# Performance work log

Measured on AMD Instinct MI355X. Metric: run time of the kernel, lower is better.

The kernel has to match this reference:

```python
import jax, jax.numpy as jnp
import numpy as np

B, S, D, H = 2, 2048, 1024, 16
DK = D // H
NEG = -1e9


def setup_inputs() -> dict:
    key = jax.random.key(0)
    ks = jax.random.split(key, 12)
    inp = {
        "query": jax.random.normal(ks[0], (B, S, D), jnp.float32),
        "key": jax.random.normal(ks[1], (B, S, D), jnp.float32),
        "value": jax.random.normal(ks[2], (B, S, D), jnp.float32),
        "mask": jax.random.randint(ks[3], (B, S), 0, 2, jnp.int32),
    }
    # 4 linears (q, k, v, out), each d_model x d_model with bias.
    scale = 1.0 / np.sqrt(D)
    for i, name in enumerate(["wq", "wk", "wv", "wo"]):
        inp[name] = jax.random.uniform(ks[4 + i], (D, D), jnp.float32, -scale, scale)
        inp["b" + name[1]] = jax.random.uniform(ks[8 + i], (D,), jnp.float32, -scale, scale)
    return inp


def _split_heads(x):  # [B,S,D] -> [B,H,S,DK]
    return x.reshape(B, S, H, DK).transpose(0, 2, 1, 3)


def reference(query, key, value, mask, wq, bq, wk, bk, wv, bv, wo, bo):
    q = _split_heads(query @ wq.T + bq)
    k = _split_heads(key @ wk.T + bk)
    v = _split_heads(value @ wv.T + bv)
    scores = jnp.einsum("bhqd,bhkd->bhqk", q, k) / jnp.sqrt(jnp.float32(DK))
    # mask: [B,S] -> [B,1,1,S]; masked_fill where mask == 0
    m = mask[:, None, None, :]
    scores = jnp.where(m == 0, NEG, scores)
    attn = jax.nn.softmax(scores, axis=-1)  # dropout p=0 (eval) -> identity
    x = jnp.einsum("bhqk,bhkd->bhqd", attn, v)
    x = x.transpose(0, 2, 1, 3).reshape(B, S, D)
    return x @ wo.T + bo
```

## Files before the change

kernel.cpp:

```cpp
#include <hip/hip_runtime.h>


typedef _Float16 f16;
typedef _Float16 f16x8 __attribute__((ext_vector_type(8)));
typedef _Float16 f16x4 __attribute__((ext_vector_type(4)));
typedef __fp16 fp16x2r __attribute__((ext_vector_type(2)));
typedef float f32x4 __attribute__((ext_vector_type(4)));
typedef float f32x16 __attribute__((ext_vector_type(16)));
typedef unsigned u32x2 __attribute__((ext_vector_type(2)));

#define MFMA_F16(a, b, c) __builtin_amdgcn_mfma_f32_16x16x32_f16((a), (b), (c), 0, 0, 0)
#define MFMA32(a, b, c) __builtin_amdgcn_mfma_f32_32x32x16_f16((a), (b), (c), 0, 0, 0)
#define L2E 1.44269504088896340736f

__device__ __forceinline__ void gld16(const void* g, void* l) {
    __builtin_amdgcn_global_load_lds(
        (__attribute__((address_space(1))) void*)(g),
        (__attribute__((address_space(3))) void*)(l), 16, 0, 0);
}

__device__ __forceinline__ void swap_halves(unsigned& a, unsigned& b) {
#if __has_builtin(__builtin_amdgcn_permlane32_swap)
    u32x2 r = __builtin_amdgcn_permlane32_swap(a, b, false, false);
    a = r[0];
    b = r[1];
#else
    unsigned pa = (unsigned)__shfl_xor((int)a, 32);
    unsigned pb = (unsigned)__shfl_xor((int)b, 32);
    if ((threadIdx.x & 32) == 0) { b = pa; } else { a = pb; }
#endif
}

__global__ __launch_bounds__(256) void cvt_kernel(
    const float* __restrict__ q, const float* __restrict__ k,
    const float* __restrict__ v,
    const float* __restrict__ wq, const float* __restrict__ wk,
    const float* __restrict__ wv, const float* __restrict__ wo,
    f16* __restrict__ oq, f16* __restrict__ ok, f16* __restrict__ ov,
    f16* __restrict__ owq, f16* __restrict__ owk, f16* __restrict__ owv,
    f16* __restrict__ owo)
{
    const int z = blockIdx.y;
    const float* src;
    f16* dst;
    int n;
    switch (z) {
        case 0: src = q;  dst = oq;  n = 4194304; break;
        case 1: src = k;  dst = ok;  n = 4194304; break;
        case 2: src = v;  dst = ov;  n = 4194304; break;
        case 3: src = wq; dst = owq; n = 1048576; break;
        case 4: src = wk; dst = owk; n = 1048576; break;
        case 5: src = wv; dst = owv; n = 1048576; break;
        default: src = wo; dst = owo; n = 1048576; break;
    }
    int idx = (blockIdx.x * 256 + threadIdx.x) * 8;
    if (idx >= n) return;
    float4 a = *(const float4*)(src + idx);
    float4 b = *(const float4*)(src + idx + 4);
    f16x8 h = { (f16)a.x, (f16)a.y, (f16)a.z, (f16)a.w,
                (f16)b.x, (f16)b.y, (f16)b.z, (f16)b.w };
    *(f16x8*)(dst + idx) = h;
}

__global__ __launch_bounds__(256) void proj_qkv_kernel(
    const f16* __restrict__ xq, const f16* __restrict__ xk,
    const f16* __restrict__ xv,
    const f16* __restrict__ wqh, const f16* __restrict__ wkh,
    const f16* __restrict__ wvh,
    const float* __restrict__ bq, const float* __restrict__ bk,
    const float* __restrict__ bv,
    f16* __restrict__ qh, f16* __restrict__ kh, f16* __restrict__ vt)
{
    const int z = blockIdx.z;
    const f16* X = (z == 0) ? xq : (z == 1) ? xk : xv;
    const f16* W = (z == 0) ? wqh : (z == 1) ? wkh : wvh;
    const float* bias = (z == 0) ? bq : (z == 1) ? bk : bv;
    const f16* P0 = (z < 2) ? W : X;
    const f16* P1 = (z < 2) ? X : W;

    __shared__ __align__(16) f16 smem[16384];
    f16* As = smem;
    f16* Bs = smem + 8192;
    f16* L  = smem;

    const int t = threadIdx.x;
    const int wave = t >> 6, lane = t & 63, quad = lane >> 4, l15 = lane & 15;
    const int m_base = (wave >> 1) * 64, n_base = (wave & 1) * 64;
    const int blockM = (z < 2) ? blockIdx.y * 128 : blockIdx.x * 128;
    const int blockN = (z < 2) ? blockIdx.x * 128 : blockIdx.y * 128;

    const int srow = lane >> 3;
    const int sblk = (lane & 7) ^ srow;

    f32x4 acc[4][4];
#pragma unroll
    for (int mt = 0; mt < 4; mt++)
#pragma unroll
        for (int nt = 0; nt < 4; nt++)
            acc[mt][nt] = (f32x4){0.f, 0.f, 0.f, 0.f};

    for (int k0 = 0; k0 < 1024; k0 += 64) {
        __syncthreads();
#pragma unroll
        for (int j = 0; j < 4; j++) {
            int r0 = wave * 32 + j * 8;
            gld16(&P0[(size_t)(blockM + r0 + srow) * 1024 + k0 + sblk * 8],
                  &As[r0 * 64]);
            gld16(&P1[(size_t)(blockN + r0 + srow) * 1024 + k0 + sblk * 8],
                  &Bs[r0 * 64]);
        }
        __syncthreads();

#pragma unroll
        for (int c = 0; c < 2; c++) {
            f16x8 af[4], bf[4];
#pragma unroll
            for (int mt = 0; mt < 4; mt++)
                af[mt] = *(const f16x8*)(&As[(m_base + mt * 16 + l15) * 64 +
                                             (((c * 4 + quad) ^ (l15 & 7)) << 3)]);
#pragma unroll
            for (int nt = 0; nt < 4; nt++)
                bf[nt] = *(const f16x8*)(&Bs[(n_base + nt * 16 + l15) * 64 +
                                             (((c * 4 + quad) ^ (l15 & 7)) << 3)]);
#pragma unroll
            for (int mt = 0; mt < 4; mt++)
#pragma unroll
                for (int nt = 0; nt < 4; nt++)
                    acc[mt][nt] = MFMA_F16(af[mt], bf[nt], acc[mt][nt]);
        }
    }

    if (z < 2) {
        f16* o = (z == 0) ? qh : kh;
        const float scale = (z == 0) ? 0.125f * L2E : 1.0f;
        float4 b4[4];
#pragma unroll
        for (int mt = 0; mt < 4; mt++)
            b4[mt] = *(const float4*)(&bias[blockM + m_base + mt * 16 + quad * 4]);

#pragma unroll
        for (int half = 0; half < 2; half++) {
            __syncthreads();
            if ((wave & 1) == half) {
#pragma unroll
                for (int mt = 0; mt < 4; mt++)
#pragma unroll
                    for (int nt = 0; nt < 4; nt++) {
                        f16x4 pk = {
                            (f16)((acc[mt][nt][0] + b4[mt].x) * scale),
                            (f16)((acc[mt][nt][1] + b4[mt].y) * scale),
                            (f16)((acc[mt][nt][2] + b4[mt].z) * scale),
                            (f16)((acc[mt][nt][3] + b4[mt].w) * scale) };
                        *(f16x4*)(&L[(nt * 16 + l15) * 136 +
                                     m_base + mt * 16 + quad * 4]) = pk;
                    }
            }
            __syncthreads();
#pragma unroll
            for (int pass = 0; pass < 4; pass++) {
                int unit = pass * 32 + (t >> 3);
                int hh = unit >> 6, s_loc = unit & 63;
                f16x8 vv = *(const f16x8*)(&L[s_loc * 136 + hh * 64 + (t & 7) * 8]);
                int s_glob = blockN + half * 64 + s_loc;
                int b = s_glob >> 11, s = s_glob & 2047;
                int h_glob = (blockM >> 6) + hh;
                *(f16x8*)(&o[(((size_t)(b * 16 + h_glob) * 2048 + s) << 6) +
                             (t & 7) * 8]) = vv;
            }
        }
    } else {
        float bv_[4];
#pragma unroll
        for (int nt = 0; nt < 4; nt++)
            bv_[nt] = bias[blockN + n_base + nt * 16 + l15];

#pragma unroll
        for (int half = 0; half < 2; half++) {
            __syncthreads();
            if ((wave & 1) == half) {
#pragma unroll
                for (int mt = 0; mt < 4; mt++)
#pragma unroll
                    for (int nt = 0; nt < 4; nt++) {
                        f16x4 pk = { (f16)(acc[mt][nt][0] + bv_[nt]),
                                     (f16)(acc[mt][nt][1] + bv_[nt]),
                                     (f16)(acc[mt][nt][2] + bv_[nt]),
                                     (f16)(acc[mt][nt][3] + bv_[nt]) };
                        *(f16x4*)(&L[(nt * 16 + l15) * 136 +
                                     m_base + mt * 16 + quad * 4]) = pk;
                    }
            }
            __syncthreads();
#pragma unroll
            for (int pass = 0; pass < 4; pass++) {
                int f_loc = pass * 16 + (t >> 4);
                f16x8 vv = *(const f16x8*)(&L[f_loc * 136 + (t & 15) * 8]);
                int feat = blockN + half * 64 + f_loc;
                int hh = feat >> 6, dk = feat & 63;
                int b = blockM >> 11;
                int s0 = (blockM & 2047) + (t & 15) * 8;
                *(f16x8*)(&vt[((size_t)((b * 16 + hh) * 64 + dk) << 11) + s0]) = vv;
            }
        }
    }
}

__device__ __forceinline__ void flash_stage(
    const f16* kbase, const f16* vbase, int key0,
    f16* Kb, f16* Vb, int wave, int srow8, int sblk)
{
#pragma unroll
    for (int p = 0; p < 2; p++) {
        int r0 = p * 32 + wave * 8;
        int row = r0 + srow8;
        gld16(&kbase[(size_t)(key0 + row) * 64 + sblk * 8], &Kb[r0 * 64]);
        gld16(&vbase[(size_t)row * 2048 + key0 + sblk * 8], &Vb[r0 * 64]);
    }
}

__device__ __forceinline__ void flash_phase(
    const f16* Kbuf, const f16* Vbuf, const float* bias_all, int key0,
    const f16x8 (&qf)[4], int l31, int hi, int hb, int l7,
    f32x16& O0, f32x16& O1, float& rs)
{
    f32x16 S[2];
#pragma unroll
    for (int mb = 0; mb < 2; mb++) {
        const float* bp = &bias_all[key0 + mb * 32 + hb];
        float4 b0 = *(const float4*)(bp);
        float4 b1 = *(const float4*)(bp + 8);
        float4 b2 = *(const float4*)(bp + 16);
        float4 b3 = *(const float4*)(bp + 24);
        S[mb] = (f32x16){b0.x, b0.y, b0.z, b0.w, b1.x, b1.y, b1.z, b1.w,
                         b2.x, b2.y, b2.z, b2.w, b3.x, b3.y, b3.z, b3.w};
    }
#pragma unroll
    for (int kc = 0; kc < 4; kc++) {
        int pb = ((kc * 2 + hi) ^ l7) << 3;
        f16x8 kf0 = *(const f16x8*)(&Kbuf[l31 * 64 + pb]);
        f16x8 kf1 = *(const f16x8*)(&Kbuf[(32 + l31) * 64 + pb]);
        S[0] = MFMA32(kf0, qf[kc], S[0]);
        S[1] = MFMA32(kf1, qf[kc], S[1]);
    }

    f16x8 Bf[4];
#pragma unroll
    for (int mb = 0; mb < 2; mb++) {
        unsigned w[8];
        float ls = 0.f;
#pragma unroll
        for (int g = 0; g < 4; g++) {
            float p0 = exp2f(S[mb][4 * g + 0]);
            float p1 = exp2f(S[mb][4 * g + 1]);
            float p2 = exp2f(S[mb][4 * g + 2]);
            float p3 = exp2f(S[mb][4 * g + 3]);
            ls += (p0 + p1) + (p2 + p3);
            union { fp16x2r h; unsigned u; } c0, c1;
            c0.h = __builtin_amdgcn_cvt_pkrtz(p0, p1);
            c1.h = __builtin_amdgcn_cvt_pkrtz(p2, p3);
            w[2 * g] = c0.u;
            w[2 * g + 1] = c1.u;
        }
        rs += ls;
        swap_halves(w[0], w[2]);
        swap_halves(w[1], w[3]);
        swap_halves(w[4], w[6]);
        swap_halves(w[5], w[7]);
        union { f16x8 v; unsigned q[4]; } bb0, bb1;
        bb0.q[0] = w[0]; bb0.q[1] = w[1]; bb0.q[2] = w[2]; bb0.q[3] = w[3];
        bb1.q[0] = w[4]; bb1.q[1] = w[5]; bb1.q[2] = w[6]; bb1.q[3] = w[7];
        Bf[2 * mb] = bb0.v;
        Bf[2 * mb + 1] = bb1.v;
    }

#pragma unroll
    for (int kc = 0; kc < 4; kc++) {
        int pb = ((kc * 2 + hi) ^ l7) << 3;
        f16x8 vf0 = *(const f16x8*)(&Vbuf[l31 * 64 + pb]);
        f16x8 vf1 = *(const f16x8*)(&Vbuf[(32 + l31) * 64 + pb]);
        O0 = MFMA32(vf0, Bf[kc], O0);
        O1 = MFMA32(vf1, Bf[kc], O1);
    }
}

__global__ __launch_bounds__(256) void flash_kernel(
    const f16* __restrict__ qh, const f16* __restrict__ kh,
    const f16* __restrict__ vt, const int* __restrict__ mask,
    f16* __restrict__ ctx)
{
    __shared__ __align__(16) f16 Ks0[64 * 64];
    __shared__ __align__(16) f16 Ks1[64 * 64];
    __shared__ __align__(16) f16 Vts0[64 * 64];
    __shared__ __align__(16) f16 Vts1[64 * 64];
    __shared__ float bias_all[2048];

    const int t = threadIdx.x;
    const int wave = t >> 6, lane = t & 63;
    const int l31 = lane & 31, hi = lane >> 5, hb = hi * 4, l7 = l31 & 7;
    const int bh = blockIdx.x;
    const int b = bh >> 4, h = bh & 15;
    const int q0 = blockIdx.y * 128;

    const f16* qbase = qh + (size_t)bh * (2048 * 64);
    const f16* kbase = kh + (size_t)bh * (2048 * 64);
    const f16* vbase = vt + (size_t)bh * (64 * 2048);

#pragma unroll
    for (int j = 0; j < 8; j++) {
        int i = j * 256 + t;
        bias_all[i] = (mask[b * 2048 + i] == 0) ? -1.0e9f : 0.0f;
    }

    const int qrow = q0 + wave * 32 + l31;
    f16x8 qf[4];
#pragma unroll
    for (int kc = 0; kc < 4; kc++)
        qf[kc] = *(const f16x8*)(&qbase[(size_t)qrow * 64 + kc * 16 + hi * 8]);

    f32x16 O0{}, O1{};
    float rs = 0.f;

    const int srow8 = lane >> 3;
    const int sblk = (lane & 7) ^ srow8;

    flash_stage(kbase, vbase, 0, Ks0, Vts0, wave, srow8, sblk);

    for (int k2 = 0; k2 < 16; k2++) {
        const int key0 = k2 * 128;
        __syncthreads();
        flash_stage(kbase, vbase, key0 + 64, Ks1, Vts1, wave, srow8, sblk);
        flash_phase(Ks0, Vts0, bias_all, key0, qf, l31, hi, hb, l7, O0, O1, rs);
        __syncthreads();
        if (k2 < 15)
            flash_stage(kbase, vbase, key0 + 128, Ks0, Vts0, wave, srow8, sblk);
        flash_phase(Ks1, Vts1, bias_all, key0 + 64, qf, l31, hi, hb, l7, O0, O1, rs);
    }

    const float l = rs + __shfl_xor(rs, 32);
    const float inv_l = 1.0f / l;

    f16* cb = &ctx[(size_t)(b * 2048 + qrow) * 1024 + h * 64];
#pragma unroll
    for (int g = 0; g < 4; g++) {
        f16x4 pk0 = { (f16)(O0[4 * g + 0] * inv_l), (f16)(O0[4 * g + 1] * inv_l),
                      (f16)(O0[4 * g + 2] * inv_l), (f16)(O0[4 * g + 3] * inv_l) };
        f16x4 pk1 = { (f16)(O1[4 * g + 0] * inv_l), (f16)(O1[4 * g + 1] * inv_l),
                      (f16)(O1[4 * g + 2] * inv_l), (f16)(O1[4 * g + 3] * inv_l) };
        *(f16x4*)(&cb[8 * g + hb]) = pk0;
        *(f16x4*)(&cb[32 + 8 * g + hb]) = pk1;
    }
}

__global__ __launch_bounds__(256) void proj_out_kernel(
    const f16* __restrict__ ctx, const f16* __restrict__ woh,
    const float* __restrict__ bo, float* __restrict__ out)
{
    __shared__ __align__(16) f16 As[2][128 * 64];
    __shared__ __align__(16) f16 Bs[2][64 * 64];

    const int t = threadIdx.x;
    const int wave = t >> 6, lane = t & 63, quad = lane >> 4, l15 = lane & 15;
    const int m_base = (wave >> 1) * 64, n_base = (wave & 1) * 32;
    const int blockM = blockIdx.x * 128;
    const int blockN = blockIdx.y * 64;

    const int srow = lane >> 3;
    const int sblk = (lane & 7) ^ srow;

    f32x4 acc[4][2];
#pragma unroll
    for (int mt = 0; mt < 4; mt++)
#pragma unroll
        for (int nt = 0; nt < 2; nt++)
            acc[mt][nt] = (f32x4){0.f, 0.f, 0.f, 0.f};

#pragma unroll
    for (int j = 0; j < 4; j++) {
        int r0 = wave * 32 + j * 8;
        gld16(&ctx[(size_t)(blockM + r0 + srow) * 1024 + sblk * 8],
              &As[0][r0 * 64]);
    }
#pragma unroll
    for (int j = 0; j < 2; j++) {
        int r0 = wave * 16 + j * 8;
        gld16(&woh[(size_t)(blockN + r0 + srow) * 1024 + sblk * 8],
              &Bs[0][r0 * 64]);
    }

    for (int ki = 0; ki < 16; ki++) {
        const int cur = ki & 1;
        __syncthreads();

        if (ki < 15) {
            const int k0n = (ki + 1) * 64;
#pragma unroll
            for (int j = 0; j < 4; j++) {
                int r0 = wave * 32 + j * 8;
                gld16(&ctx[(size_t)(blockM + r0 + srow) * 1024 + k0n + sblk * 8],
                      &As[cur ^ 1][r0 * 64]);
            }
#pragma unroll
            for (int j = 0; j < 2; j++) {
                int r0 = wave * 16 + j * 8;
                gld16(&woh[(size_t)(blockN + r0 + srow) * 1024 + k0n + sblk * 8],
                      &Bs[cur ^ 1][r0 * 64]);
            }
        }

#pragma unroll
        for (int c = 0; c < 2; c++) {
            f16x8 af[4], bf[2];
#pragma unroll
            for (int mt = 0; mt < 4; mt++)
                af[mt] = *(const f16x8*)(&As[cur][(m_base + mt * 16 + l15) * 64 +
                                              (((c * 4 + quad) ^ (l15 & 7)) << 3)]);
#pragma unroll
            for (int nt = 0; nt < 2; nt++)
                bf[nt] = *(const f16x8*)(&Bs[cur][(n_base + nt * 16 + l15) * 64 +
                                              (((c * 4 + quad) ^ (l15 & 7)) << 3)]);
#pragma unroll
            for (int mt = 0; mt < 4; mt++)
#pragma unroll
                for (int nt = 0; nt < 2; nt++)
                    acc[mt][nt] = MFMA_F16(af[mt], bf[nt], acc[mt][nt]);
        }
    }

    float bo_[2];
#pragma unroll
    for (int nt = 0; nt < 2; nt++)
        bo_[nt] = bo[blockN + n_base + nt * 16 + l15];

#pragma unroll
    for (int mt = 0; mt < 4; mt++) {
        int row0 = blockM + m_base + mt * 16 + quad * 4;
#pragma unroll
        for (int nt = 0; nt < 2; nt++) {
            int col_g = blockN + n_base + nt * 16 + l15;
#pragma unroll
            for (int i = 0; i < 4; i++)
                out[(size_t)(row0 + i) * 1024 + col_g] = acc[mt][nt][i] + bo_[nt];
        }
    }
}

extern "C" void kernel_launch(void* const* d_in, const int* in_sizes, int n_in,
                              void* d_out, int out_size, void* d_ws, size_t ws_size,
                              hipStream_t stream) {
    const float* query = (const float*)d_in[0];
    const float* key_  = (const float*)d_in[1];
    const float* value = (const float*)d_in[2];
    const int*   mask  = (const int*)d_in[3];
    const float* wq = (const float*)d_in[4];
    const float* bq = (const float*)d_in[5];
    const float* wk = (const float*)d_in[6];
    const float* bk = (const float*)d_in[7];
    const float* wv = (const float*)d_in[8];
    const float* bv = (const float*)d_in[9];
    const float* wo = (const float*)d_in[10];
    const float* bo = (const float*)d_in[11];
    float* out = (float*)d_out;

    f16* xq  = (f16*)d_ws;
    f16* xk  = xq  + 4194304;
    f16* xv  = xk  + 4194304;
    f16* wqh = xv  + 4194304;
    f16* wkh = wqh + 1048576;
    f16* wvh = wkh + 1048576;
    f16* woh = wvh + 1048576;
    f16* qh  = woh + 1048576;
    f16* kh  = qh  + 4194304;
    f16* vt  = kh  + 4194304;
    f16* ctx = xq;

    cvt_kernel<<<dim3(2048, 7), 256, 0, stream>>>(
        query, key_, value, wq, wk, wv, wo, xq, xk, xv, wqh, wkh, wvh, woh);
    proj_qkv_kernel<<<dim3(32, 8, 3), 256, 0, stream>>>(
        xq, xk, xv, wqh, wkh, wvh, bq, bk, bv, qh, kh, vt);
    flash_kernel<<<dim3(32, 16), 256, 0, stream>>>(qh, kh, vt, mask, ctx);
    proj_out_kernel<<<dim3(32, 16), 256, 0, stream>>>(ctx, woh, bo, out);
}
```

Baseline: 237.1 us.

## Split attention keys across two blocks and merge partials in a combine kernel

```diff
diff --git a/kernel.cpp b/kernel.cpp
--- a/kernel.cpp
+++ b/kernel.cpp
@@ -219,14 +219,14 @@
 }
 
 __device__ __forceinline__ void flash_phase(
-    const f16* Kbuf, const f16* Vbuf, const float* bias_all, int key0,
+    const f16* Kbuf, const f16* Vbuf, const float* bias_loc, int key0,
     const f16x8 (&qf)[4], int l31, int hi, int hb, int l7,
     f32x16& O0, f32x16& O1, float& rs)
 {
     f32x16 S[2];
 #pragma unroll
     for (int mb = 0; mb < 2; mb++) {
-        const float* bp = &bias_all[key0 + mb * 32 + hb];
+        const float* bp = &bias_loc[key0 + mb * 32 + hb];
         float4 b0 = *(const float4*)(bp);
         float4 b1 = *(const float4*)(bp + 8);
         float4 b2 = *(const float4*)(bp + 16);
@@ -286,13 +286,13 @@
 __global__ __launch_bounds__(256) void flash_kernel(
     const f16* __restrict__ qh, const f16* __restrict__ kh,
     const f16* __restrict__ vt, const int* __restrict__ mask,
-    f16* __restrict__ ctx)
+    f16* __restrict__ opart, float* __restrict__ lpart)
 {
     __shared__ __align__(16) f16 Ks0[64 * 64];
     __shared__ __align__(16) f16 Ks1[64 * 64];
     __shared__ __align__(16) f16 Vts0[64 * 64];
     __shared__ __align__(16) f16 Vts1[64 * 64];
-    __shared__ float bias_all[2048];
+    __shared__ float bias_loc[1024];
 
     const int t = threadIdx.x;
     const int wave = t >> 6, lane = t & 63;
@@ -300,15 +300,17 @@
     const int bh = blockIdx.x;
     const int b = bh >> 4, h = bh & 15;
     const int q0 = blockIdx.y * 128;
+    const int sp = blockIdx.z;
+    const int key_base = sp * 1024;
 
     const f16* qbase = qh + (size_t)bh * (2048 * 64);
-    const f16* kbase = kh + (size_t)bh * (2048 * 64);
-    const f16* vbase = vt + (size_t)bh * (64 * 2048);
-
-#pragma unroll
-    for (int j = 0; j < 8; j++) {
+    const f16* kbase = kh + (size_t)bh * (2048 * 64) + (size_t)key_base * 64;
+    const f16* vbase = vt + (size_t)bh * (64 * 2048) + key_base;
+
+#pragma unroll
+    for (int j = 0; j < 4; j++) {
         int i = j * 256 + t;
-        bias_all[i] = (mask[b * 2048 + i] == 0) ? -1.0e9f : 0.0f;
+        bias_loc[i] = (mask[b * 2048 + key_base + i] == 0) ? -1.0e9f : 0.0f;
     }
 
     const int qrow = q0 + wave * 32 + l31;
@@ -325,30 +327,54 @@
 
     flash_stage(kbase, vbase, 0, Ks0, Vts0, wave, srow8, sblk);
 
-    for (int k2 = 0; k2 < 16; k2++) {
+    for (int k2 = 0; k2 < 8; k2++) {
         const int key0 = k2 * 128;
         __syncthreads();
         flash_stage(kbase, vbase, key0 + 64, Ks1, Vts1, wave, srow8, sblk);
-        flash_phase(Ks0, Vts0, bias_all, key0, qf, l31, hi, hb, l7, O0, O1, rs);
+        flash_phase(Ks0, Vts0, bias_loc, key0, qf, l31, hi, hb, l7, O0, O1, rs);
         __syncthreads();
-        if (k2 < 15)
+        if (k2 < 7)
             flash_stage(kbase, vbase, key0 + 128, Ks0, Vts0, wave, srow8, sblk);
-        flash_phase(Ks1, Vts1, bias_all, key0 + 64, qf, l31, hi, hb, l7, O0, O1, rs);
-    }
-
-    const float l = rs + __shfl_xor(rs, 32);
-    const float inv_l = 1.0f / l;
-
-    f16* cb = &ctx[(size_t)(b * 2048 + qrow) * 1024 + h * 64];
+        flash_phase(Ks1, Vts1, bias_loc, key0 + 64, qf, l31, hi, hb, l7, O0, O1, rs);
+    }
+
+    const float l_scaled = (rs + __shfl_xor(rs, 32)) * 0.00390625f;
+    if (hi == 0)
+        lpart[sp * 65536 + bh * 2048 + qrow] = l_scaled;
+
+    f16* ob = &opart[(size_t)sp * 4194304 +
+                     (size_t)(b * 2048 + qrow) * 1024 + h * 64];
+    const float sc = 0.00390625f;
 #pragma unroll
     for (int g = 0; g < 4; g++) {
-        f16x4 pk0 = { (f16)(O0[4 * g + 0] * inv_l), (f16)(O0[4 * g + 1] * inv_l),
-                      (f16)(O0[4 * g + 2] * inv_l), (f16)(O0[4 * g + 3] * inv_l) };
-        f16x4 pk1 = { (f16)(O1[4 * g + 0] * inv_l), (f16)(O1[4 * g + 1] * inv_l),
-                      (f16)(O1[4 * g + 2] * inv_l), (f16)(O1[4 * g + 3] * inv_l) };
-        *(f16x4*)(&cb[8 * g + hb]) = pk0;
-        *(f16x4*)(&cb[32 + 8 * g + hb]) = pk1;
-    }
+        f16x4 pk0 = { (f16)(O0[4 * g + 0] * sc), (f16)(O0[4 * g + 1] * sc),
+                      (f16)(O0[4 * g + 2] * sc), (f16)(O0[4 * g + 3] * sc) };
+        f16x4 pk1 = { (f16)(O1[4 * g + 0] * sc), (f16)(O1[4 * g + 1] * sc),
+                      (f16)(O1[4 * g + 2] * sc), (f16)(O1[4 * g + 3] * sc) };
+        *(f16x4*)(&ob[8 * g + hb]) = pk0;
+        *(f16x4*)(&ob[32 + 8 * g + hb]) = pk1;
+    }
+}
+
+__global__ __launch_bounds__(256) void combine_kernel(
+    const f16* __restrict__ opart, const float* __restrict__ lpart,
+    f16* __restrict__ ctx)
+{
+    int idx = (blockIdx.x * 256 + threadIdx.x) * 8;
+    int token = idx >> 10;
+    int feat = idx & 1023;
+    int b = token >> 11, s = token & 2047;
+    int h = feat >> 6;
+    float la = lpart[(b * 16 + h) * 2048 + s];
+    float lb = lpart[65536 + (b * 16 + h) * 2048 + s];
+    float inv = 1.0f / (la + lb);
+    f16x8 a = *(const f16x8*)(opart + idx);
+    f16x8 bb = *(const f16x8*)(opart + 4194304 + idx);
+    f16x8 r;
+#pragma unroll
+    for (int i = 0; i < 8; i++)
+        r[i] = (f16)(((float)a[i] + (float)bb[i]) * inv);
+    *(f16x8*)(ctx + idx) = r;
 }
 
 __global__ __launch_bounds__(256) void proj_out_kernel(
@@ -471,12 +497,15 @@
     f16* qh  = woh + 1048576;
     f16* kh  = qh  + 4194304;
     f16* vt  = kh  + 4194304;
-    f16* ctx = xq;
+    f16* ctx   = xq;
+    f16* opart = xk;
+    float* lp  = (float*)wqh;
 
     cvt_kernel<<<dim3(2048, 7), 256, 0, stream>>>(
         query, key_, value, wq, wk, wv, wo, xq, xk, xv, wqh, wkh, wvh, woh);
     proj_qkv_kernel<<<dim3(32, 8, 3), 256, 0, stream>>>(
         xq, xk, xv, wqh, wkh, wvh, bq, bk, bv, qh, kh, vt);
-    flash_kernel<<<dim3(32, 16), 256, 0, stream>>>(qh, kh, vt, mask, ctx);
+    flash_kernel<<<dim3(32, 16, 2), 256, 0, stream>>>(qh, kh, vt, mask, opart, lp);
+    combine_kernel<<<dim3(2048), 256, 0, stream>>>(opart, lp, ctx);
     proj_out_kernel<<<dim3(32, 16), 256, 0, stream>>>(ctx, woh, bo, out);
 }
```

After: 248.5 us. 1.05x slower.
